# Kernel optimization log

Hardware: AMD Instinct MI355X
Metric: run time of the kernel (lower is better)

The kernel has to match this reference:

```python
import jax, jax.numpy as jnp
import numpy as np

BN_EPS = 1e-5
LRELU_SLOPE = 0.2


def setup_inputs() -> dict:
    key = jax.random.key(0)
    ks = jax.random.split(key, 8)
    B, N, D = 32, 2048, 64      # batch, nodes per graph, latent_dim
    E = 1_000_000               # num edges
    H = 128                     # edge_hidden_dim
    Din = 2 * D + 4             # concat(z_src, z_dst, edge_attr)
    z = jax.random.normal(ks[0], (B, N, D), dtype=jnp.float32)
    edge_index = jax.random.randint(ks[1], (2, E), 0, B * N, dtype=jnp.int64)
    edge_attr = jax.random.normal(ks[2], (E, 4), dtype=jnp.float32)
    W1 = jax.random.normal(ks[3], (Din, H), dtype=jnp.float32) * (1.0 / np.sqrt(Din))
    b1 = jnp.zeros((H,), dtype=jnp.float32)
    gamma = jnp.ones((H,), dtype=jnp.float32)
    beta = jnp.zeros((H,), dtype=jnp.float32)
    W2 = jax.random.normal(ks[4], (H, 1), dtype=jnp.float32) * (1.0 / np.sqrt(H))
    b2 = jnp.zeros((1,), dtype=jnp.float32)
    return {"z": z, "edge_attr": edge_attr, "W1": W1, "b1": b1,
            "gamma": gamma, "beta": beta, "W2": W2, "b2": b2,
            "edge_index": edge_index}


def reference(z, edge_attr, W1, b1, gamma, beta, W2, b2, edge_index):
    B, N, D = z.shape
    zf = z.reshape(-1, D)                       # [B*N, D]
    src, dst = edge_index[0], edge_index[1]
    edge_batch = jnp.clip(src // N, 0, B - 1)
    edge_offsets = edge_batch * N               # batch_offsets[edge_batch]
    src_idx = src % N + edge_offsets
    dst_idx = dst % N + edge_offsets
    edge_input = jnp.concatenate([zf[src_idx], zf[dst_idx], edge_attr], axis=1)  # [E, 2D+4]
    h = edge_input @ W1 + b1                    # [E, H]
    # BatchNorm1d (training mode: biased batch stats over edge dim)
    mu = jnp.mean(h, axis=0)
    var = jnp.mean(jnp.square(h - mu), axis=0)
    h = (h - mu) * jax.lax.rsqrt(var + BN_EPS) * gamma + beta
    h = jnp.where(h >= 0, h, LRELU_SLOPE * h)   # LeakyReLU(0.2)
    return h @ W2 + b2                          # [E, 1]
```

## Files before the change

### kernel.cpp

```cpp
#include <hip/hip_runtime.h>

#define E_EDGES   1000000
#define NNODES    2048
#define DLAT      64
#define HCH       128
#define KP        168
#define TILE      64
#define NTILES    (E_EDGES / TILE)
#define NSPREAD   8
#define GRID_GEMM 2048
#define ZVEC      (32 * 2048 * 64 / 4)
#define ZBLK      2048

typedef short  shortx8 __attribute__((ext_vector_type(8)));
typedef float  floatx4 __attribute__((ext_vector_type(4)));

__device__ __forceinline__ unsigned short f2bf(float f) {
  union { float f; unsigned int u; } v; v.f = f;
  unsigned int r = (v.u + 0x7fffu + ((v.u >> 16) & 1u)) >> 16;
  return (unsigned short)r;
}

__device__ __forceinline__ void cfence() { asm volatile("" ::: "memory"); }
__device__ __forceinline__ void bar_lds() {
  asm volatile("s_waitcnt lgkmcnt(0)" ::: "memory");
  __builtin_amdgcn_s_barrier();
  cfence();
}

__global__ void k_prep(const float* __restrict__ z, const float* __restrict__ W1,
                       const float* __restrict__ b1,
                       unsigned short* __restrict__ zb, unsigned short* __restrict__ w1t,
                       float* __restrict__ gstats) {
  int bid = blockIdx.x;
  if (bid < ZBLK) {
    const float4* z4 = (const float4*)z;
    ushort4* zb4 = (ushort4*)zb;
    for (int i = bid * 256 + threadIdx.x; i < ZVEC; i += ZBLK * 256) {
      float4 v = z4[i];
      ushort4 o;
      o.x = f2bf(v.x); o.y = f2bf(v.y); o.z = f2bf(v.z); o.w = f2bf(v.w);
      zb4[i] = o;
    }
  } else if (bid == ZBLK) {
    for (int idx = threadIdx.x; idx < 132 * HCH; idx += 256) {
      int k = idx >> 7, n = idx & 127;
      w1t[n * KP + k] = f2bf(W1[idx]);
    }
    for (int idx = threadIdx.x; idx < HCH * (KP - 132); idx += 256) {
      int n = idx / (KP - 132);
      int k = 132 + (idx - n * (KP - 132));
      w1t[n * KP + k] = (k == 132) ? f2bf(b1[n]) : (unsigned short)0;
    }
  } else {
    for (int i = threadIdx.x; i < NSPREAD * 2 * HCH; i += 256) gstats[i] = 0.f;
  }
}

template<bool OUT>
__global__ __launch_bounds__(256, 2)
void k_gemm(const unsigned short* __restrict__ zb,
            const unsigned short* __restrict__ w1t,
            const int* __restrict__ ei,
            const float* __restrict__ attr,
            float* __restrict__ gstats,
            const float* __restrict__ gamma,
            const float* __restrict__ beta,
            const float* __restrict__ W2,
            const float* __restrict__ b2,
            float* __restrict__ out) {
  __shared__ __align__(16) unsigned short A[2 * TILE * KP];
  __shared__ float s_sum[HCH], s_sq[HCH];
  __shared__ float po[TILE];

  const int tid  = threadIdx.x;
  const int lane = tid & 63;
  const int wave = tid >> 6;
  const int l15  = lane & 15;
  const int quad = lane >> 4;
  const int eh   = wave >> 1;
  const int nh   = wave & 1;
  const int e    = tid >> 2;
  const int q    = tid & 3;
  const int grid = GRID_GEMM;

  shortx8 bfr[4][5];
#pragma unroll
  for (int nt = 0; nt < 4; ++nt) {
    const unsigned short* bp = w1t + (nh * 64 + nt * 16 + l15) * KP + quad * 8;
#pragma unroll
    for (int kk = 0; kk < 5; ++kk)
      bfr[nt][kk] = *(const shortx8*)(bp + kk * 32);
  }

  float ea[4], ebb[4], ew2[4], b2v = 0.f;
  float ssum[4] = {0.f, 0.f, 0.f, 0.f}, ssq[4] = {0.f, 0.f, 0.f, 0.f};
  if (OUT) {
#pragma unroll
    for (int nt = 0; nt < 4; ++nt) {
      int c = nh * 64 + nt * 16 + l15;
      float S = 0.f, Q = 0.f;
#pragma unroll
      for (int i = 0; i < NSPREAD; ++i) {
        S += gstats[i * 2 * HCH + c];
        Q += gstats[i * 2 * HCH + HCH + c];
      }
      float mu   = S * (1.0f / (float)E_EDGES);
      float var  = Q * (1.0f / (float)E_EDGES) - mu * mu;
      float rstd = rsqrtf(var + 1e-5f);
      float a = gamma[c] * rstd;
      ea[nt]  = a;
      ebb[nt] = beta[c] - mu * a;
      ew2[nt] = W2[c];
    }
    b2v = b2[0];
  } else {
    if (tid < HCH) { s_sum[tid] = 0.f; s_sq[tid] = 0.f; }
  }

  {
    ushort4 bl; bl.x = 0x3F80; bl.y = 0; bl.z = 0; bl.w = 0;
    uint4 zed = {0, 0, 0, 0};
#pragma unroll
    for (int b = 0; b < 2; ++b) {
      unsigned short* rp = A + b * (TILE * KP) + e * KP;
      if (q == 0) *(ushort4*)(rp + 132) = bl;
      *(uint4*)(rp + 136 + q * 8) = zed;
    }
  }

  const int t0 = blockIdx.x;
  int tc1 = t0 + grid;  if (tc1 > NTILES - 1) tc1 = NTILES - 1;
  int tc2 = tc1 + grid; if (tc2 > NTILES - 1) tc2 = NTILES - 1;

  uint4 g0, g1, g2, g3;
  float4 av;
  int s2, d2;
  {
    int s0 = ei[t0 * TILE + e];
    int d0 = ei[E_EDGES + t0 * TILE + e];
    int r0 = (q < 2) ? s0 : ((s0 & ~(NNODES - 1)) | (d0 & (NNODES - 1)));
    const uint4* sp = (const uint4*)(zb + r0 * DLAT + (q & 1) * 32);
    g0 = sp[0]; g1 = sp[1]; g2 = sp[2]; g3 = sp[3];
    if (wave == 0) av = ((const float4*)attr)[t0 * TILE + tid];
    s2 = ei[tc1 * TILE + e];
    d2 = ei[E_EDGES + tc1 * TILE + e];
    uint4* dst = (uint4*)(A + e * KP + q * 32);
    dst[0] = g0; dst[1] = g1; dst[2] = g2; dst[3] = g3;
    if (wave == 0) {
      ushort4 a0; a0.x = f2bf(av.x); a0.y = f2bf(av.y); a0.z = f2bf(av.z); a0.w = f2bf(av.w);
      *(ushort4*)(A + tid * KP + 128) = a0;
    }
    int r1 = (q < 2) ? s2 : ((s2 & ~(NNODES - 1)) | (d2 & (NNODES - 1)));
    const uint4* sp1 = (const uint4*)(zb + r1 * DLAT + (q & 1) * 32);
    g0 = sp1[0]; g1 = sp1[1]; g2 = sp1[2]; g3 = sp1[3];
    if (wave == 0) av = ((const float4*)attr)[tc1 * TILE + tid];
    s2 = ei[tc2 * TILE + e];
    d2 = ei[E_EDGES + tc2 * TILE + e];
  }
  bar_lds();

  int pp = 0;
  for (int tile = t0; ; ) {
    const unsigned short* Ar = A + pp * (TILE * KP);

    floatx4 acc[2][4];
#pragma unroll
    for (int mt = 0; mt < 2; ++mt)
#pragma unroll
      for (int nt = 0; nt < 4; ++nt)
        acc[mt][nt] = (floatx4){0.f, 0.f, 0.f, 0.f};

#pragma unroll
    for (int kk = 0; kk < 5; ++kk) {
      shortx8 afr[2];
#pragma unroll
      for (int mt = 0; mt < 2; ++mt)
        afr[mt] = *(const shortx8*)(Ar + (eh * 32 + mt * 16 + l15) * KP + kk * 32 + quad * 8);
#pragma unroll
      for (int mt = 0; mt < 2; ++mt)
#pragma unroll
        for (int nt = 0; nt < 4; ++nt)
          acc[mt][nt] = __builtin_amdgcn_mfma_f32_16x16x32_bf16(
              afr[mt], bfr[nt][kk], acc[mt][nt], 0, 0, 0);
    }

    const int tnext = tile + grid;
    const bool more = tnext < NTILES;
    if (more) {
      unsigned short* Aw = A + (pp ^ 1) * (TILE * KP);
      uint4* dst = (uint4*)(Aw + e * KP + q * 32);
      dst[0] = g0; dst[1] = g1; dst[2] = g2; dst[3] = g3;
      if (wave == 0) {
        ushort4 a0; a0.x = f2bf(av.x); a0.y = f2bf(av.y); a0.z = f2bf(av.z); a0.w = f2bf(av.w);
        *(ushort4*)(Aw + tid * KP + 128) = a0;
      }
      int tn1 = tnext + grid; if (tn1 > NTILES - 1) tn1 = NTILES - 1;
      int tn2 = tn1 + grid;  if (tn2 > NTILES - 1) tn2 = NTILES - 1;
      int r = (q < 2) ? s2 : ((s2 & ~(NNODES - 1)) | (d2 & (NNODES - 1)));
      const uint4* sp = (const uint4*)(zb + r * DLAT + (q & 1) * 32);
      g0 = sp[0]; g1 = sp[1]; g2 = sp[2]; g3 = sp[3];
      if (wave == 0) av = ((const float4*)attr)[tn1 * TILE + tid];
      s2 = ei[tn2 * TILE + e];
      d2 = ei[E_EDGES + tn2 * TILE + e];
    }

    if (!OUT) {
#pragma unroll
      for (int nt = 0; nt < 4; ++nt) {
        float s = 0.f, qq = 0.f;
#pragma unroll
        for (int mt = 0; mt < 2; ++mt)
#pragma unroll
          for (int r = 0; r < 4; ++r) {
            float h = acc[mt][nt][r];
            s += h; qq += h * h;
          }
        ssum[nt] += s; ssq[nt] += qq;
      }
    } else {
      float tpart[2][4];
#pragma unroll
      for (int mt = 0; mt < 2; ++mt)
#pragma unroll
        for (int r = 0; r < 4; ++r) {
          float t = 0.f;
#pragma unroll
          for (int nt = 0; nt < 4; ++nt) {
            float h = acc[mt][nt][r];
            float p = ea[nt] * h + ebb[nt];
            p = (p >= 0.f) ? p : 0.2f * p;
            t += p * ew2[nt];
          }
          t += __shfl_xor(t, 1);
          t += __shfl_xor(t, 2);
          t += __shfl_xor(t, 4);
          t += __shfl_xor(t, 8);
          tpart[mt][r] = t;
        }
      if (nh == 1 && l15 == 0) {
#pragma unroll
        for (int mt = 0; mt < 2; ++mt)
#pragma unroll
          for (int r = 0; r < 4; ++r)
            po[eh * 32 + mt * 16 + quad * 4 + r] = tpart[mt][r];
      }
      bar_lds();
      if (nh == 0 && l15 == 0) {
#pragma unroll
        for (int mt = 0; mt < 2; ++mt)
#pragma unroll
          for (int r = 0; r < 4; ++r) {
            int el = eh * 32 + mt * 16 + quad * 4 + r;
            out[tile * TILE + el] = tpart[mt][r] + po[el] + b2v;
          }
      }
    }

    if (!more) break;
    bar_lds();
    pp ^= 1;
    tile = tnext;
  }

  if (!OUT) {
#pragma unroll
    for (int nt = 0; nt < 4; ++nt) {
      float s = ssum[nt], qq = ssq[nt];
      s += __shfl_xor(s, 16); s += __shfl_xor(s, 32);
      qq += __shfl_xor(qq, 16); qq += __shfl_xor(qq, 32);
      if (quad == 0) {
        atomicAdd(&s_sum[nh * 64 + nt * 16 + l15], s);
        atomicAdd(&s_sq [nh * 64 + nt * 16 + l15], qq);
      }
    }
    __syncthreads();
    float* dstc = gstats + (blockIdx.x & (NSPREAD - 1)) * 2 * HCH;
    if (tid < HCH)          atomicAdd(&dstc[tid], s_sum[tid]);
    else if (tid < 2 * HCH) atomicAdd(&dstc[tid], s_sq[tid - HCH]);
  }
}

extern "C" void kernel_launch(void* const* d_in, const int* in_sizes, int n_in,
                              void* d_out, int out_size, void* d_ws, size_t ws_size,
                              hipStream_t stream) {
  const float* z     = (const float*)d_in[0];
  const float* attr  = (const float*)d_in[1];
  const float* W1    = (const float*)d_in[2];
  const float* b1    = (const float*)d_in[3];
  const float* gamma = (const float*)d_in[4];
  const float* beta  = (const float*)d_in[5];
  const float* W2    = (const float*)d_in[6];
  const float* b2    = (const float*)d_in[7];
  const int*   ei    = (const int*)d_in[8];
  float* out = (float*)d_out;

  char* ws = (char*)d_ws;
  unsigned short* zb  = (unsigned short*)ws;
  unsigned short* w1t = (unsigned short*)(ws + 8388608);
  float* gstats       = (float*)(ws + 8431616);

  k_prep<<<ZBLK + 2, 256, 0, stream>>>(z, W1, b1, zb, w1t, gstats);
  k_gemm<false><<<GRID_GEMM, 256, 0, stream>>>(zb, w1t, ei, attr, gstats,
                                               gamma, beta, W2, b2, nullptr);
  k_gemm<true><<<GRID_GEMM, 256, 0, stream>>>(zb, w1t, ei, attr, gstats,
                                              gamma, beta, W2, b2, out);
}
```

Before: 241.3 us.

## Shrink LDS row pitch to raise occupancy and merge per-tile barriers

Reduces the padded K pitch of the staged A tile and the transposed W1 from 168 to 136. The last MFMA k-step now has quad 0 read the 8 real columns and the other quads read a shared zero pad, instead of every quad reading zeroed columns. With the smaller LDS footprint, launch bounds rise to 3 blocks per CU. The output partials are double-buffered by ping-pong index so the two per-tile barriers merge into one. The intent is higher occupancy for latency hiding of the gathers; the risks are register pressure under the tighter bound and bank conflicts from the new pitch.

```diff
diff --git a/kernel.cpp b/kernel.cpp
--- a/kernel.cpp
+++ b/kernel.cpp
@@ -4,7 +4,7 @@
 #define NNODES    2048
 #define DLAT      64
 #define HCH       128
-#define KP        168
+#define KP        136
 #define TILE      64
 #define NTILES    (E_EDGES / TILE)
 #define NSPREAD   8
@@ -58,7 +58,7 @@
 }
 
 template<bool OUT>
-__global__ __launch_bounds__(256, 2)
+__global__ __launch_bounds__(256, 3)
 void k_gemm(const unsigned short* __restrict__ zb,
             const unsigned short* __restrict__ w1t,
             const int* __restrict__ ei,
@@ -70,8 +70,9 @@
             const float* __restrict__ b2,
             float* __restrict__ out) {
   __shared__ __align__(16) unsigned short A[2 * TILE * KP];
+  __shared__ __align__(16) unsigned short zpad[8];
   __shared__ float s_sum[HCH], s_sq[HCH];
-  __shared__ float po[TILE];
+  __shared__ float po[2][TILE];
 
   const int tid  = threadIdx.x;
   const int lane = tid & 63;
@@ -89,8 +90,10 @@
   for (int nt = 0; nt < 4; ++nt) {
     const unsigned short* bp = w1t + (nh * 64 + nt * 16 + l15) * KP + quad * 8;
 #pragma unroll
-    for (int kk = 0; kk < 5; ++kk)
+    for (int kk = 0; kk < 4; ++kk)
       bfr[nt][kk] = *(const shortx8*)(bp + kk * 32);
+    bfr[nt][4] = (quad == 0) ? *(const shortx8*)(bp - quad * 8 + 128)
+                             : (shortx8){0,0,0,0,0,0,0,0};
   }
 
   float ea[4], ebb[4], ew2[4], b2v = 0.f;
@@ -118,15 +121,13 @@
     if (tid < HCH) { s_sum[tid] = 0.f; s_sq[tid] = 0.f; }
   }
 
-  {
+  if (tid < 128) {
+    int b = tid >> 6, r = tid & 63;
     ushort4 bl; bl.x = 0x3F80; bl.y = 0; bl.z = 0; bl.w = 0;
+    *(ushort4*)(A + b * (TILE * KP) + r * KP + 132) = bl;
+  } else if (tid == 128) {
     uint4 zed = {0, 0, 0, 0};
-#pragma unroll
-    for (int b = 0; b < 2; ++b) {
-      unsigned short* rp = A + b * (TILE * KP) + e * KP;
-      if (q == 0) *(ushort4*)(rp + 132) = bl;
-      *(uint4*)(rp + 136 + q * 8) = zed;
-    }
+    *(uint4*)zpad = zed;
   }
 
   const int t0 = blockIdx.x;
@@ -175,8 +176,13 @@
     for (int kk = 0; kk < 5; ++kk) {
       shortx8 afr[2];
 #pragma unroll
-      for (int mt = 0; mt < 2; ++mt)
-        afr[mt] = *(const shortx8*)(Ar + (eh * 32 + mt * 16 + l15) * KP + kk * 32 + quad * 8);
+      for (int mt = 0; mt < 2; ++mt) {
+        const unsigned short* ap =
+            (kk < 4) ? (Ar + (eh * 32 + mt * 16 + l15) * KP + kk * 32 + quad * 8)
+                     : ((quad == 0) ? (Ar + (eh * 32 + mt * 16 + l15) * KP + 128)
+                                    : zpad);
+        afr[mt] = *(const shortx8*)ap;
+      }
 #pragma unroll
       for (int mt = 0; mt < 2; ++mt)
 #pragma unroll
@@ -205,6 +211,7 @@
       d2 = ei[E_EDGES + tn2 * TILE + e];
     }
 
+    float tpart[2][4];
     if (!OUT) {
 #pragma unroll
       for (int nt = 0; nt < 4; ++nt) {
@@ -219,7 +226,6 @@
         ssum[nt] += s; ssq[nt] += qq;
       }
     } else {
-      float tpart[2][4];
 #pragma unroll
       for (int mt = 0; mt < 2; ++mt)
 #pragma unroll
@@ -243,22 +249,23 @@
         for (int mt = 0; mt < 2; ++mt)
 #pragma unroll
           for (int r = 0; r < 4; ++r)
-            po[eh * 32 + mt * 16 + quad * 4 + r] = tpart[mt][r];
-      }
-      bar_lds();
-      if (nh == 0 && l15 == 0) {
-#pragma unroll
-        for (int mt = 0; mt < 2; ++mt)
-#pragma unroll
-          for (int r = 0; r < 4; ++r) {
-            int el = eh * 32 + mt * 16 + quad * 4 + r;
-            out[tile * TILE + el] = tpart[mt][r] + po[el] + b2v;
-          }
-      }
+            po[pp][eh * 32 + mt * 16 + quad * 4 + r] = tpart[mt][r];
+      }
+    }
+
+    bar_lds();
+
+    if (OUT && nh == 0 && l15 == 0) {
+#pragma unroll
+      for (int mt = 0; mt < 2; ++mt)
+#pragma unroll
+        for (int r = 0; r < 4; ++r) {
+          int el = eh * 32 + mt * 16 + quad * 4 + r;
+          out[tile * TILE + el] = tpart[mt][r] + po[pp][el] + b2v;
+        }
     }
 
     if (!more) break;
-    bar_lds();
     pp ^= 1;
     tile = tnext;
   }
@@ -298,7 +305,7 @@
   char* ws = (char*)d_ws;
   unsigned short* zb  = (unsigned short*)ws;
   unsigned short* w1t = (unsigned short*)(ws + 8388608);
-  float* gstats       = (float*)(ws + 8431616);
+  float* gstats       = (float*)(ws + 8423424);
 
   k_prep<<<ZBLK + 2, 256, 0, stream>>>(z, W1, b1, zb, w1t, gstats);
   k_gemm<false><<<GRID_GEMM, 256, 0, stream>>>(zb, w1t, ei, attr, gstats,
```

Result: slower. 309.5 us (+28.3%).

## Bin edges by batch into packed records and shrink K padding in GEMM

Applied to the files above, without the earlier changes.

Adds a histogram and a scatter pass that sort edges into 8 bins by the top bits of the source index. Each edge is written as a 16-byte record holding both row indices, the bf16 edge attributes and the original edge id. The two GEMM passes then read these records, so node-row gathers land in smaller regions of the bf16 z copy and should hit cache more often, and each edge needs one load instead of separate index and attr loads. K padding is cut from 168 to 136, with the last K chunk handled by an MFMA where only quad 0 supplies data. The main loop is reordered to use one barrier per tile. The cost is an extra kernel, a memset and the record traffic, and outputs are now written scattered through the original edge id.

```diff
diff --git a/kernel.cpp b/kernel.cpp
--- a/kernel.cpp
+++ b/kernel.cpp
@@ -2,15 +2,19 @@
 
 #define E_EDGES   1000000
 #define NNODES    2048
-#define DLAT      64
 #define HCH       128
-#define KP        168
+#define KP        136
 #define TILE      64
 #define NTILES    (E_EDGES / TILE)
 #define NSPREAD   8
 #define GRID_GEMM 2048
 #define ZVEC      (32 * 2048 * 64 / 4)
 #define ZBLK      2048
+#define WBLK      66
+#define HBLK      128
+#define NBIN      8
+#define NRUN      3907
+#define SBLK      977
 
 typedef short  shortx8 __attribute__((ext_vector_type(8)));
 typedef float  floatx4 __attribute__((ext_vector_type(4)));
@@ -20,18 +24,22 @@
   unsigned int r = (v.u + 0x7fffu + ((v.u >> 16) & 1u)) >> 16;
   return (unsigned short)r;
 }
-
 __device__ __forceinline__ void cfence() { asm volatile("" ::: "memory"); }
 __device__ __forceinline__ void bar_lds() {
   asm volatile("s_waitcnt lgkmcnt(0)" ::: "memory");
   __builtin_amdgcn_s_barrier();
   cfence();
 }
+__device__ __forceinline__ unsigned pack_rows(int s, int d) {
+  unsigned rs = (unsigned)s & 0xFFFFu;
+  unsigned rd = (unsigned)(((s & ~(NNODES - 1)) | (d & (NNODES - 1)))) & 0xFFFFu;
+  return rs | (rd << 16);
+}
 
 __global__ void k_prep(const float* __restrict__ z, const float* __restrict__ W1,
-                       const float* __restrict__ b1,
+                       const float* __restrict__ b1, const int* __restrict__ ei,
                        unsigned short* __restrict__ zb, unsigned short* __restrict__ w1t,
-                       float* __restrict__ gstats) {
+                       float* __restrict__ gstats, int* __restrict__ hist) {
   int bid = blockIdx.x;
   if (bid < ZBLK) {
     const float4* z4 = (const float4*)z;
@@ -42,36 +50,110 @@
       o.x = f2bf(v.x); o.y = f2bf(v.y); o.z = f2bf(v.z); o.w = f2bf(v.w);
       zb4[i] = o;
     }
-  } else if (bid == ZBLK) {
-    for (int idx = threadIdx.x; idx < 132 * HCH; idx += 256) {
-      int k = idx >> 7, n = idx & 127;
-      w1t[n * KP + k] = f2bf(W1[idx]);
-    }
-    for (int idx = threadIdx.x; idx < HCH * (KP - 132); idx += 256) {
-      int n = idx / (KP - 132);
-      int k = 132 + (idx - n * (KP - 132));
-      w1t[n * KP + k] = (k == 132) ? f2bf(b1[n]) : (unsigned short)0;
-    }
+  } else if (bid < ZBLK + WBLK) {
+    int idx = (bid - ZBLK) * 256 + threadIdx.x;
+    int k = idx >> 7, n = idx & 127;
+    w1t[n * KP + k] = f2bf(W1[idx]);
+  } else if (bid == ZBLK + WBLK) {
+    int tid = threadIdx.x;
+    if (tid < 512) {
+      int n = tid >> 2, kp = 132 + (tid & 3);
+      w1t[n * KP + kp] = (kp == 132) ? f2bf(b1[n]) : (unsigned short)0;
+    }
+    for (int i = tid; i < NSPREAD * 2 * HCH; i += 256) gstats[i] = 0.f;
   } else {
-    for (int i = threadIdx.x; i < NSPREAD * 2 * HCH; i += 256) gstats[i] = 0.f;
-  }
+    __shared__ int lh[NBIN];
+    int tid = threadIdx.x;
+    if (tid < NBIN) lh[tid] = 0;
+    __syncthreads();
+    int hb = bid - (ZBLK + WBLK + 1);
+    for (int e = hb * 256 + tid; e < E_EDGES; e += HBLK * 256)
+      atomicAdd(&lh[((unsigned)ei[e]) >> 13], 1);
+    __syncthreads();
+    if (tid < NBIN) atomicAdd(&hist[tid], lh[tid]);
+  }
+}
+
+__global__ __launch_bounds__(256)
+void k_scatter(const int* __restrict__ ei, const float* __restrict__ attr,
+               const int* __restrict__ hist, int* __restrict__ cur,
+               uint4* __restrict__ recs) {
+  __shared__ int spfx[NBIN];
+  if (threadIdx.x == 0) {
+    int a = 0;
+    for (int b = 0; b < NBIN; ++b) { spfx[b] = a; a += hist[b]; }
+  }
+  __syncthreads();
+  const int wid  = blockIdx.x * 4 + (threadIdx.x >> 6);
+  const int lane = threadIdx.x & 63;
+  if (wid >= NRUN) return;
+  const int e0 = wid * 256;
+
+  int s[4], d[4], bin[4];
+  float4 at[4];
+  bool val[4];
+#pragma unroll
+  for (int k = 0; k < 4; ++k) {
+    int e = e0 + k * 64 + lane;
+    val[k] = (e < E_EDGES);
+    if (val[k]) {
+      s[k] = ei[e];
+      d[k] = ei[E_EDGES + e];
+      at[k] = ((const float4*)attr)[e];
+      bin[k] = ((unsigned)s[k]) >> 13;
+    } else bin[k] = -1;
+  }
+
+  int slot[4];
+  const unsigned long long below = (lane == 63) ? ~0ull >> 1
+                                 : ((1ull << (lane + 1)) - 1) >> 1;
+#pragma unroll
+  for (int bb = 0; bb < NBIN; ++bb) {
+    unsigned long long m[4];
+    int pre[4], tot = 0;
+#pragma unroll
+    for (int k = 0; k < 4; ++k) {
+      m[k] = __ballot(bin[k] == bb);
+      pre[k] = tot;
+      tot += __popcll(m[k]);
+    }
+    int base = 0;
+    if (tot) {
+      if (lane == 0) base = atomicAdd(&cur[bb], tot);
+      base = __shfl(base, 0);
+#pragma unroll
+      for (int k = 0; k < 4; ++k)
+        if (bin[k] == bb)
+          slot[k] = spfx[bb] + base + pre[k] + __popcll(m[k] & below);
+    }
+  }
+
+#pragma unroll
+  for (int k = 0; k < 4; ++k)
+    if (val[k]) {
+      uint4 r;
+      r.x = pack_rows(s[k], d[k]);
+      r.y = (unsigned)f2bf(at[k].x) | ((unsigned)f2bf(at[k].y) << 16);
+      r.z = (unsigned)f2bf(at[k].z) | ((unsigned)f2bf(at[k].w) << 16);
+      r.w = (unsigned)(e0 + k * 64 + lane);
+      recs[slot[k]] = r;
+    }
 }
 
 template<bool OUT>
 __global__ __launch_bounds__(256, 2)
 void k_gemm(const unsigned short* __restrict__ zb,
             const unsigned short* __restrict__ w1t,
-            const int* __restrict__ ei,
-            const float* __restrict__ attr,
+            const uint4* __restrict__ recs,
             float* __restrict__ gstats,
             const float* __restrict__ gamma,
             const float* __restrict__ beta,
             const float* __restrict__ W2,
             const float* __restrict__ b2,
             float* __restrict__ out) {
-  __shared__ __align__(16) unsigned short A[2 * TILE * KP];
+  __shared__ __align__(16) unsigned short A[2][TILE * KP];
   __shared__ float s_sum[HCH], s_sq[HCH];
-  __shared__ float po[TILE];
+  __shared__ float po[2][TILE];
 
   const int tid  = threadIdx.x;
   const int lane = tid & 63;
@@ -84,13 +166,15 @@
   const int q    = tid & 3;
   const int grid = GRID_GEMM;
 
-  shortx8 bfr[4][5];
+  shortx8 bfr[4][4], bfr4[4];
 #pragma unroll
   for (int nt = 0; nt < 4; ++nt) {
-    const unsigned short* bp = w1t + (nh * 64 + nt * 16 + l15) * KP + quad * 8;
-#pragma unroll
-    for (int kk = 0; kk < 5; ++kk)
-      bfr[nt][kk] = *(const shortx8*)(bp + kk * 32);
+    const unsigned short* bp = w1t + (nh * 64 + nt * 16 + l15) * KP;
+#pragma unroll
+    for (int kk = 0; kk < 4; ++kk)
+      bfr[nt][kk] = *(const shortx8*)(bp + kk * 32 + quad * 8);
+    bfr4[nt] = (quad == 0) ? *(const shortx8*)(bp + 128)
+                           : (shortx8){0, 0, 0, 0, 0, 0, 0, 0};
   }
 
   float ea[4], ebb[4], ew2[4], b2v = 0.f;
@@ -118,52 +202,47 @@
     if (tid < HCH) { s_sum[tid] = 0.f; s_sq[tid] = 0.f; }
   }
 
+  auto stage = [&](uint4 rec, const uint4* g, int buf) {
+    uint4* dst = (uint4*)(&A[buf][0] + e * KP + q * 32);
+    dst[0] = g[0]; dst[1] = g[1]; dst[2] = g[2]; dst[3] = g[3];
+    if (q == 0) {
+      ushort4 av; av.x = (unsigned short)rec.y; av.y = (unsigned short)(rec.y >> 16);
+      av.z = (unsigned short)rec.z; av.w = (unsigned short)(rec.z >> 16);
+      *(ushort4*)(&A[buf][0] + e * KP + 128) = av;
+      ushort4 bl; bl.x = 0x3F80; bl.y = 0; bl.z = 0; bl.w = 0;
+      *(ushort4*)(&A[buf][0] + e * KP + 132) = bl;
+    }
+  };
+  auto gather = [&](uint4 rec, uint4* g) {
+    unsigned row = (q < 2) ? (rec.x & 0xFFFFu) : (rec.x >> 16);
+    const uint4* sp = (const uint4*)(zb + (size_t)row * 64 + (q & 1) * 32);
+    g[0] = sp[0]; g[1] = sp[1]; g[2] = sp[2]; g[3] = sp[3];
+  };
+
+  const int t0 = blockIdx.x;
+  uint4 recN, g[4];
   {
-    ushort4 bl; bl.x = 0x3F80; bl.y = 0; bl.z = 0; bl.w = 0;
-    uint4 zed = {0, 0, 0, 0};
-#pragma unroll
-    for (int b = 0; b < 2; ++b) {
-      unsigned short* rp = A + b * (TILE * KP) + e * KP;
-      if (q == 0) *(ushort4*)(rp + 132) = bl;
-      *(uint4*)(rp + 136 + q * 8) = zed;
-    }
-  }
-
-  const int t0 = blockIdx.x;
-  int tc1 = t0 + grid;  if (tc1 > NTILES - 1) tc1 = NTILES - 1;
-  int tc2 = tc1 + grid; if (tc2 > NTILES - 1) tc2 = NTILES - 1;
-
-  uint4 g0, g1, g2, g3;
-  float4 av;
-  int s2, d2;
-  {
-    int s0 = ei[t0 * TILE + e];
-    int d0 = ei[E_EDGES + t0 * TILE + e];
-    int r0 = (q < 2) ? s0 : ((s0 & ~(NNODES - 1)) | (d0 & (NNODES - 1)));
-    const uint4* sp = (const uint4*)(zb + r0 * DLAT + (q & 1) * 32);
-    g0 = sp[0]; g1 = sp[1]; g2 = sp[2]; g3 = sp[3];
-    if (wave == 0) av = ((const float4*)attr)[t0 * TILE + tid];
-    s2 = ei[tc1 * TILE + e];
-    d2 = ei[E_EDGES + tc1 * TILE + e];
-    uint4* dst = (uint4*)(A + e * KP + q * 32);
-    dst[0] = g0; dst[1] = g1; dst[2] = g2; dst[3] = g3;
-    if (wave == 0) {
-      ushort4 a0; a0.x = f2bf(av.x); a0.y = f2bf(av.y); a0.z = f2bf(av.z); a0.w = f2bf(av.w);
-      *(ushort4*)(A + tid * KP + 128) = a0;
-    }
-    int r1 = (q < 2) ? s2 : ((s2 & ~(NNODES - 1)) | (d2 & (NNODES - 1)));
-    const uint4* sp1 = (const uint4*)(zb + r1 * DLAT + (q & 1) * 32);
-    g0 = sp1[0]; g1 = sp1[1]; g2 = sp1[2]; g3 = sp1[3];
-    if (wave == 0) av = ((const float4*)attr)[tc1 * TILE + tid];
-    s2 = ei[tc2 * TILE + e];
-    d2 = ei[E_EDGES + tc2 * TILE + e];
+    uint4 recA = recs[t0 * TILE + e];
+    gather(recA, g);
+    stage(recA, g, 0);
+    recN = recs[(t0 + grid) * TILE + e];
+    gather(recN, g);
   }
   bar_lds();
 
-  int pp = 0;
+  int pp = 0, sl = 0;
   for (int tile = t0; ; ) {
-    const unsigned short* Ar = A + pp * (TILE * KP);
-
+    const int tnext = tile + grid;
+    const bool more = tnext < NTILES;
+
+    uint4 recF;
+    if (more) {
+      stage(recN, g, pp ^ 1);
+      int tC = tile + 2 * grid; if (tC > NTILES - 1) tC = NTILES - 1;
+      recF = recs[tC * TILE + e];
+    }
+
+    const unsigned short* Ar = &A[pp][0];
     floatx4 acc[2][4];
 #pragma unroll
     for (int mt = 0; mt < 2; ++mt)
@@ -172,7 +251,7 @@
         acc[mt][nt] = (floatx4){0.f, 0.f, 0.f, 0.f};
 
 #pragma unroll
-    for (int kk = 0; kk < 5; ++kk) {
+    for (int kk = 0; kk < 4; ++kk) {
       shortx8 afr[2];
 #pragma unroll
       for (int mt = 0; mt < 2; ++mt)
@@ -184,27 +263,24 @@
           acc[mt][nt] = __builtin_amdgcn_mfma_f32_16x16x32_bf16(
               afr[mt], bfr[nt][kk], acc[mt][nt], 0, 0, 0);
     }
-
-    const int tnext = tile + grid;
-    const bool more = tnext < NTILES;
-    if (more) {
-      unsigned short* Aw = A + (pp ^ 1) * (TILE * KP);
-      uint4* dst = (uint4*)(Aw + e * KP + q * 32);
-      dst[0] = g0; dst[1] = g1; dst[2] = g2; dst[3] = g3;
-      if (wave == 0) {
-        ushort4 a0; a0.x = f2bf(av.x); a0.y = f2bf(av.y); a0.z = f2bf(av.z); a0.w = f2bf(av.w);
-        *(ushort4*)(Aw + tid * KP + 128) = a0;
-      }
-      int tn1 = tnext + grid; if (tn1 > NTILES - 1) tn1 = NTILES - 1;
-      int tn2 = tn1 + grid;  if (tn2 > NTILES - 1) tn2 = NTILES - 1;
-      int r = (q < 2) ? s2 : ((s2 & ~(NNODES - 1)) | (d2 & (NNODES - 1)));
-      const uint4* sp = (const uint4*)(zb + r * DLAT + (q & 1) * 32);
-      g0 = sp[0]; g1 = sp[1]; g2 = sp[2]; g3 = sp[3];
-      if (wave == 0) av = ((const float4*)attr)[tn1 * TILE + tid];
-      s2 = ei[tn2 * TILE + e];
-      d2 = ei[E_EDGES + tn2 * TILE + e];
-    }
-
+    {
+      shortx8 a4[2];
+#pragma unroll
+      for (int mt = 0; mt < 2; ++mt)
+        a4[mt] = (quad == 0)
+            ? *(const shortx8*)(Ar + (eh * 32 + mt * 16 + l15) * KP + 128)
+            : (shortx8){0, 0, 0, 0, 0, 0, 0, 0};
+#pragma unroll
+      for (int mt = 0; mt < 2; ++mt)
+#pragma unroll
+        for (int nt = 0; nt < 4; ++nt)
+          acc[mt][nt] = __builtin_amdgcn_mfma_f32_16x16x32_bf16(
+              a4[mt], bfr4[nt], acc[mt][nt], 0, 0, 0);
+    }
+
+    if (more) gather(recF, g);
+
+    float tpart[2][4];
     if (!OUT) {
 #pragma unroll
       for (int nt = 0; nt < 4; ++nt) {
@@ -219,7 +295,6 @@
         ssum[nt] += s; ssq[nt] += qq;
       }
     } else {
-      float tpart[2][4];
 #pragma unroll
       for (int mt = 0; mt < 2; ++mt)
 #pragma unroll
@@ -243,23 +318,26 @@
         for (int mt = 0; mt < 2; ++mt)
 #pragma unroll
           for (int r = 0; r < 4; ++r)
-            po[eh * 32 + mt * 16 + quad * 4 + r] = tpart[mt][r];
+            po[sl][eh * 32 + mt * 16 + quad * 4 + r] = tpart[mt][r];
       }
-      bar_lds();
-      if (nh == 0 && l15 == 0) {
-#pragma unroll
-        for (int mt = 0; mt < 2; ++mt)
-#pragma unroll
-          for (int r = 0; r < 4; ++r) {
-            int el = eh * 32 + mt * 16 + quad * 4 + r;
-            out[tile * TILE + el] = tpart[mt][r] + po[el] + b2v;
-          }
-      }
+    }
+
+    bar_lds();
+
+    if (OUT && nh == 0 && l15 == 0) {
+#pragma unroll
+      for (int mt = 0; mt < 2; ++mt)
+#pragma unroll
+        for (int r = 0; r < 4; ++r) {
+          int el = eh * 32 + mt * 16 + quad * 4 + r;
+          int orig = ((const int*)recs)[(tile * TILE + el) * 4 + 3];
+          out[orig] = tpart[mt][r] + po[sl][el] + b2v;
+        }
     }
 
     if (!more) break;
-    bar_lds();
-    pp ^= 1;
+    recN = recF;
+    pp ^= 1; sl ^= 1;
     tile = tnext;
   }
 
@@ -298,11 +376,17 @@
   char* ws = (char*)d_ws;
   unsigned short* zb  = (unsigned short*)ws;
   unsigned short* w1t = (unsigned short*)(ws + 8388608);
-  float* gstats       = (float*)(ws + 8431616);
-
-  k_prep<<<ZBLK + 2, 256, 0, stream>>>(z, W1, b1, zb, w1t, gstats);
-  k_gemm<false><<<GRID_GEMM, 256, 0, stream>>>(zb, w1t, ei, attr, gstats,
+  float* gstats       = (float*)(ws + 8423424);
+  int* hist           = (int*)(ws + 8431616);
+  int* cur            = (int*)(ws + 8431648);
+  uint4* recs         = (uint4*)(ws + 8431680);
+
+  hipMemsetAsync(ws + 8431616, 0, 64, stream);
+  k_prep<<<ZBLK + WBLK + 1 + HBLK, 256, 0, stream>>>(z, W1, b1, ei, zb, w1t,
+                                                     gstats, hist);
+  k_scatter<<<SBLK, 256, 0, stream>>>(ei, attr, hist, cur, recs);
+  k_gemm<false><<<GRID_GEMM, 256, 0, stream>>>(zb, w1t, recs, gstats,
                                                gamma, beta, W2, b2, nullptr);
-  k_gemm<true><<<GRID_GEMM, 256, 0, stream>>>(zb, w1t, ei, attr, gstats,
+  k_gemm<true><<<GRID_GEMM, 256, 0, stream>>>(zb, w1t, recs, gstats,
                                               gamma, beta, W2, b2, out);
 }
```

Measured after the change: 675.8 us. 2.8x slower.
